# Kernel tuning notes

Hardware: AMD Instinct MI355X
Metric: run time of the kernel (lower is better)

Reference implementation:

```python
import jax, jax.numpy as jnp
import numpy as np

N_FEAT = 27  # 26 embeddings + bot MLP output
LI = np.array([i for i in range(N_FEAT) for j in range(i)])
LJ = np.array([j for i in range(N_FEAT) for j in range(i)])


def _mlp(x, Ws, bs):
    for W, b in zip(Ws, bs):
        x = jax.nn.relu(x @ W + b)
    return x


def setup_inputs() -> dict:
    key = jax.random.key(0)
    ks = jax.random.split(key, 32)
    B, V, D = 32768, 50000, 128
    bot = [13, 512, 256, 128]
    top = [479, 1024, 1024, 512, 256, 1]
    inp = {
        "dense_x": jax.random.normal(ks[0], (B, 13), dtype=jnp.float32),
        "sparse_x": jax.random.randint(ks[1], (B, 26), 0, V, dtype=jnp.int64),
        "emb": jax.random.normal(ks[2], (26, V, D), dtype=jnp.float32) * 0.01,
    }
    for i in range(3):
        inp[f"bw{i}"] = jax.random.normal(ks[3 + i], (bot[i], bot[i + 1]), dtype=jnp.float32) * (1.0 / np.sqrt(bot[i]))
        inp[f"bb{i}"] = jnp.zeros((bot[i + 1],), dtype=jnp.float32)
    for i in range(5):
        inp[f"tw{i}"] = jax.random.normal(ks[8 + i], (top[i], top[i + 1]), dtype=jnp.float32) * (1.0 / np.sqrt(top[i]))
        inp[f"tb{i}"] = jnp.zeros((top[i + 1],), dtype=jnp.float32)
    return inp


def reference(dense_x, sparse_x, emb,
              bw0, bb0, bw1, bb1, bw2, bb2,
              tw0, tb0, tw1, tb1, tw2, tb2, tw3, tb3, tw4, tb4):
    B = dense_x.shape[0]
    bot_out = _mlp(dense_x, [bw0, bw1, bw2], [bb0, bb1, bb2])  # [B, 128]
    # multi-table embedding gather: emb[t, sparse_x[:, t]] -> [B, 26, 128]
    gathered = jnp.take_along_axis(
        emb[None, :, :, :],  # broadcast over batch via vmap-style gather
        sparse_x.T[None, :, :, None].astype(jnp.int32) * 0, 0
    ) if False else jnp.stack(
        [emb[t][sparse_x[:, t]] for t in range(emb.shape[0])], axis=1
    )
    features = jnp.concatenate([bot_out[:, None, :], gathered], axis=1)  # [B, 27, 128]
    # batched dot interaction: [B, 27, 27], then triangular gather
    Z = jnp.einsum('bnd,bmd->bnm', features, features)
    interact = Z[:, LI, LJ]  # [B, 351]
    x = jnp.concatenate([bot_out, interact], axis=1)  # [B, 479]
    return _mlp(x, [tw0, tw1, tw2, tw3, tw4], [tb0, tb1, tb2, tb3, tb4])  # [B, 1]
```

## Files before the change

kernel.cpp:

```cpp
#include <hip/hip_runtime.h>

typedef _Float16 f16;
typedef __attribute__((ext_vector_type(2))) _Float16 f16x2;
typedef __attribute__((ext_vector_type(4))) _Float16 f16x4;
typedef __attribute__((ext_vector_type(8))) _Float16 f16x8;
typedef __attribute__((ext_vector_type(4))) float f32x4;

#define BM 128
#define BN 128
#define BK 32

#define TBM 256
#define TBN 256
#define TBK 64

__device__ __forceinline__ void gl_lds16(const void* g, void* l) {
    __builtin_amdgcn_global_load_lds(
        (const __attribute__((address_space(1))) void*)g,
        (__attribute__((address_space(3))) void*)l, 16, 0, 0);
}

struct ConvtDesc { const float* src; f16* dst; int K, N, Kpad, tileOff; };
struct ConvtArgs { ConvtDesc d[6]; };

__global__ void convt6_kernel(ConvtArgs args)
{
    __shared__ float tile[64][65];
    int bid = blockIdx.x;
    int w = 0;
    #pragma unroll
    for (int i = 1; i < 6; ++i) if (bid >= args.d[i].tileOff) w = i;
    const float* __restrict__ src = args.d[w].src;
    f16* __restrict__ dst = args.d[w].dst;
    int K = args.d[w].K, N = args.d[w].N, Kpad = args.d[w].Kpad;
    int local = bid - args.d[w].tileOff;
    int tk = Kpad >> 6;
    int k0 = (local % tk) * 64;
    int n0 = (local / tk) * 64;
    int tid = threadIdx.x;
    #pragma unroll
    for (int it = 0; it < 16; ++it) {
        int idx = it * 256 + tid;
        int kr = idx >> 6, nc = idx & 63;
        float v = 0.f;
        if (k0 + kr < K) v = src[(size_t)(k0 + kr) * N + n0 + nc];
        tile[kr][nc] = v;
    }
    __syncthreads();
    #pragma unroll
    for (int it = 0; it < 16; ++it) {
        int idx = it * 256 + tid;
        int nr = idx >> 6, kc = idx & 63;
        dst[(size_t)(n0 + nr) * Kpad + k0 + kc] = (f16)tile[kc][nr];
    }
}

__global__ void bot0_kernel(const float* __restrict__ xin, const float* __restrict__ w,
                            const float* __restrict__ bias, f16* __restrict__ out)
{
    int t = blockIdx.x * 256 + threadIdx.x;
    int b = t >> 9, n = t & 511;
    float acc = bias[n];
    #pragma unroll
    for (int k = 0; k < 13; ++k) acc += xin[b * 13 + k] * w[k * 512 + n];
    out[(size_t)b * 512 + n] = (f16)fmaxf(acc, 0.f);
}

__global__ void gemm_f16(const f16* __restrict__ A, const f16* __restrict__ WT,
                         const float* __restrict__ bias, f16* __restrict__ C,
                         int N, int K)
{
    __shared__ __align__(16) f16 lsA[BM * BK];
    __shared__ __align__(16) f16 lsB[BN * BK];
    int tid  = threadIdx.x;
    int lane = tid & 63;
    int wave = tid >> 6;
    int brow = blockIdx.y * BM;
    int bcol = blockIdx.x * BN;
    int wr = wave >> 1, wc = wave & 1;

    f32x4 acc[4][4] = {};
    int rsel = lane & 15;
    int k8   = lane >> 4;

    int nK = K / BK;
    for (int kt = 0; kt < nK; ++kt) {
        int k0 = kt * BK;
        #pragma unroll
        for (int i = 0; i < 2; ++i) {
            int flat = i * 256 + tid;
            int row  = flat >> 2;
            int slot = flat & 3;
            int sg   = slot ^ ((row >> 1) & 3);
            gl_lds16(A  + (size_t)(brow + row) * K + k0 + sg * 8, lsA + flat * 8);
            gl_lds16(WT + (size_t)(bcol + row) * K + k0 + sg * 8, lsB + flat * 8);
        }
        __syncthreads();

        f16x8 aF[4], bF[4];
        #pragma unroll
        for (int m = 0; m < 4; ++m) {
            int ra = wr * 64 + m * 16 + rsel;
            int sa = k8 ^ ((ra >> 1) & 3);
            aF[m] = *(const f16x8*)(lsA + ra * 32 + sa * 8);
        }
        #pragma unroll
        for (int n = 0; n < 4; ++n) {
            int rb = wc * 64 + n * 16 + rsel;
            int sb = k8 ^ ((rb >> 1) & 3);
            bF[n] = *(const f16x8*)(lsB + rb * 32 + sb * 8);
        }
        #pragma unroll
        for (int m = 0; m < 4; ++m)
            #pragma unroll
            for (int n = 0; n < 4; ++n)
                acc[m][n] = __builtin_amdgcn_mfma_f32_16x16x32_f16(aF[m], bF[n], acc[m][n], 0, 0, 0);
        __syncthreads();
    }

    #pragma unroll
    for (int n = 0; n < 4; ++n) {
        int col = bcol + wc * 64 + n * 16 + (lane & 15);
        float bv = bias[col];
        #pragma unroll
        for (int m = 0; m < 4; ++m) {
            int rowb = brow + wr * 64 + m * 16 + (lane >> 4) * 4;
            #pragma unroll
            for (int r = 0; r < 4; ++r) {
                float v = acc[m][n][r] + bv;
                C[(size_t)(rowb + r) * N + col] = (f16)fmaxf(v, 0.f);
            }
        }
    }
}

__global__ __launch_bounds__(512, 2) void gemm256_f16(
    const f16* __restrict__ A, const f16* __restrict__ WT,
    const float* __restrict__ bias, f16* __restrict__ C, int N, int K)
{
    __shared__ __align__(16) f16 ls[2][2 * TBM * TBK];
    int tid  = threadIdx.x;
    int lane = tid & 63;
    int wid  = tid >> 6;
    int wm = wid >> 2, wn = wid & 3;

    int nbx = gridDim.x;
    int flat = blockIdx.y * nbx + blockIdx.x;
    int nchunk = (nbx * gridDim.y) >> 3;
    int nf = (flat & 7) * nchunk + (flat >> 3);
    int bx = nf % nbx, by = nf / nbx;
    int brow = by * TBM, bcol = bx * TBN;

    f32x4 acc[8][4] = {};
    int rsel = lane & 15;
    int k8   = lane >> 4;

    const size_t szK = (size_t)K;
    auto stage = [&](int buf, int kt) {
        const f16* gA = A  + (size_t)brow * szK + kt * TBK;
        const f16* gB = WT + (size_t)bcol * szK + kt * TBK;
        f16* dA = &ls[buf][0];
        f16* dB = &ls[buf][TBM * TBK];
        #pragma unroll
        for (int i = 0; i < 4; ++i) {
            int fl  = i * 512 + tid;
            int row = fl >> 3;
            int sl  = fl & 7;
            int sg  = sl ^ (row & 7);
            gl_lds16(gA + (size_t)row * szK + sg * 8, dA + fl * 8);
            gl_lds16(gB + (size_t)row * szK + sg * 8, dB + fl * 8);
        }
    };

    int nK = K / TBK;
    stage(0, 0);
    __syncthreads();

    for (int kt = 0; kt < nK; ++kt) {
        int cur = kt & 1;
        if (kt + 1 < nK) stage(cur ^ 1, kt + 1);
        const f16* pA = &ls[cur][0];
        const f16* pB = &ls[cur][TBM * TBK];
        #pragma unroll
        for (int ks = 0; ks < 2; ++ks) {
            f16x8 aF[8], bF[4];
            #pragma unroll
            for (int m = 0; m < 8; ++m) {
                int ra = wm * 128 + m * 16 + rsel;
                int s  = (ks * 4 + k8) ^ (ra & 7);
                aF[m] = *(const f16x8*)(pA + ra * 64 + s * 8);
            }
            #pragma unroll
            for (int n = 0; n < 4; ++n) {
                int rb = wn * 64 + n * 16 + rsel;
                int s  = (ks * 4 + k8) ^ (rb & 7);
                bF[n] = *(const f16x8*)(pB + rb * 64 + s * 8);
            }
            #pragma unroll
            for (int m = 0; m < 8; ++m)
                #pragma unroll
                for (int n = 0; n < 4; ++n)
                    acc[m][n] = __builtin_amdgcn_mfma_f32_16x16x32_f16(aF[m], bF[n], acc[m][n], 0, 0, 0);
        }
        __syncthreads();
    }

    #pragma unroll
    for (int n = 0; n < 4; ++n) {
        int col = bcol + wn * 64 + n * 16 + (lane & 15);
        float bv = bias[col];
        #pragma unroll
        for (int m = 0; m < 8; ++m) {
            int rowb = brow + wm * 128 + m * 16 + (lane >> 4) * 4;
            #pragma unroll
            for (int r = 0; r < 4; ++r)
                C[(size_t)(rowb + r) * N + col] = (f16)fmaxf(acc[m][n][r] + bv, 0.f);
        }
    }
}

__global__ void interact_mfma(const f16* __restrict__ botout,
                              const float* __restrict__ emb,
                              const int* __restrict__ sparse,
                              f16* __restrict__ x, int V)
{
    __shared__ __align__(16) f16 F[4][32][128];
    __shared__ __align__(16) f16 xs[4][512];
    int tid  = threadIdx.x;
    int lane = tid & 63, wave = tid >> 6;
    int b0 = blockIdx.x * 4;

    for (int t = tid; t < 4 * 27 * 16; t += 256) {
        int s   = t / (27 * 16);
        int rem = t - s * (27 * 16);
        int r   = rem >> 4;
        int c   = rem & 15;
        int b   = b0 + s;
        f16x8 v;
        if (r == 0) {
            v = *(const f16x8*)(botout + (size_t)b * 128 + c * 8);
        } else {
            const float* src = emb + ((size_t)(r - 1) * V + sparse[b * 26 + (r - 1)]) * 128 + c * 8;
            #pragma unroll
            for (int e = 0; e < 8; ++e) v[e] = (f16)src[e];
        }
        *(f16x8*)(&F[s][r][(c ^ (r & 15)) * 8]) = v;
    }
    __syncthreads();

    f32x4 a00 = {}, a10 = {}, a11 = {};
    int rl = lane & 15, ch = lane >> 4;
    #pragma unroll
    for (int ks = 0; ks < 4; ++ks) {
        int c = ks * 4 + ch;
        f16x8 f0 = *(const f16x8*)(&F[wave][rl]     [(c ^ rl) * 8]);
        f16x8 f1 = *(const f16x8*)(&F[wave][16 + rl][(c ^ rl) * 8]);
        a00 = __builtin_amdgcn_mfma_f32_16x16x32_f16(f0, f0, a00, 0, 0, 0);
        a10 = __builtin_amdgcn_mfma_f32_16x16x32_f16(f1, f0, a10, 0, 0, 0);
        a11 = __builtin_amdgcn_mfma_f32_16x16x32_f16(f1, f1, a11, 0, 0, 0);
    }

    #pragma unroll
    for (int r = 0; r < 4; ++r) {
        int i = ch * 4 + r, j = rl;
        if (i > j) xs[wave][128 + (i * (i - 1)) / 2 + j] = (f16)a00[r];
    }
    #pragma unroll
    for (int r = 0; r < 4; ++r) {
        int i = 16 + ch * 4 + r, j = rl;
        if (i < 27) xs[wave][128 + (i * (i - 1)) / 2 + j] = (f16)a10[r];
    }
    #pragma unroll
    for (int r = 0; r < 4; ++r) {
        int i = 16 + ch * 4 + r, j = 16 + rl;
        if (i < 27 && j < i) xs[wave][128 + (i * (i - 1)) / 2 + j] = (f16)a11[r];
    }
    #pragma unroll
    for (int d = lane; d < 128; d += 64) xs[wave][d] = F[wave][0][d];
    if (lane < 33) xs[wave][479 + lane] = (f16)0;
    __syncthreads();

    {
        int b = b0 + wave;
        f16x8 v = *(const f16x8*)(&xs[wave][lane * 8]);
        *(f16x8*)(x + (size_t)b * 512 + lane * 8) = v;
    }
}

__global__ void top4_kernel(const f16* __restrict__ a, const float* __restrict__ w,
                            const float* __restrict__ bias, float* __restrict__ out)
{
    int wave = threadIdx.x >> 6, lane = threadIdx.x & 63;
    int b = blockIdx.x * 4 + wave;
    f16x4 av = *(const f16x4*)(a + (size_t)b * 256 + lane * 4);
    float acc = 0.f;
    #pragma unroll
    for (int k = 0; k < 4; ++k) acc += (float)av[k] * w[lane * 4 + k];
    #pragma unroll
    for (int off = 32; off; off >>= 1) acc += __shfl_xor(acc, off, 64);
    if (lane == 0) out[b] = fmaxf(acc + bias[0], 0.f);
}

extern "C" void kernel_launch(void* const* d_in, const int* in_sizes, int n_in,
                              void* d_out, int out_size, void* d_ws, size_t ws_size,
                              hipStream_t stream)
{
    (void)n_in; (void)out_size; (void)ws_size;
    const float* dense  = (const float*)d_in[0];
    const int*   sparse = (const int*)  d_in[1];
    const float* emb    = (const float*)d_in[2];
    const float* bw0 = (const float*)d_in[3];
    const float* bb0 = (const float*)d_in[4];
    const float* bw1 = (const float*)d_in[5];
    const float* bb1 = (const float*)d_in[6];
    const float* bw2 = (const float*)d_in[7];
    const float* bb2 = (const float*)d_in[8];
    const float* tw0 = (const float*)d_in[9];
    const float* tb0 = (const float*)d_in[10];
    const float* tw1 = (const float*)d_in[11];
    const float* tb1 = (const float*)d_in[12];
    const float* tw2 = (const float*)d_in[13];
    const float* tb2 = (const float*)d_in[14];
    const float* tw3 = (const float*)d_in[15];
    const float* tb3 = (const float*)d_in[16];
    const float* tw4 = (const float*)d_in[17];
    const float* tb4 = (const float*)d_in[18];
    float* out = (float*)d_out;

    const int B = in_sizes[0] / 13;
    const int V = in_sizes[2] / (26 * 128);

    char* ws = (char*)d_ws;
    size_t off = 0;
    auto alloc = [&](size_t bytes) {
        char* p = ws + off;
        off += (bytes + 255) & ~(size_t)255;
        return p;
    };
    f16* S1   = (f16*)alloc((size_t)B * 1024 * 2);
    f16* t1   = (f16*)alloc((size_t)B * 1024 * 2);
    f16* S3   = (f16*)alloc((size_t)B * 512 * 2);
    f16* S4   = (f16*)alloc((size_t)B * 256 * 2);
    f16* act2 = (f16*)alloc((size_t)B * 128 * 2);
    f16* bw1T = (f16*)alloc((size_t)256 * 512 * 2);
    f16* bw2T = (f16*)alloc((size_t)128 * 256 * 2);
    f16* tw0T = (f16*)alloc((size_t)1024 * 512 * 2);
    f16* tw1T = (f16*)alloc((size_t)1024 * 1024 * 2);
    f16* tw2T = (f16*)alloc((size_t)512 * 1024 * 2);
    f16* tw3T = (f16*)alloc((size_t)256 * 512 * 2);
    f16* act0 = S1; f16* t2 = S1;
    f16* x    = S3; f16* t3 = S3;
    f16* act1 = S4; f16* t4 = S4;

    ConvtArgs ca;
    ca.d[0] = { bw1, bw1T,  512,  256,  512,   0 };
    ca.d[1] = { bw2, bw2T,  256,  128,  256,  32 };
    ca.d[2] = { tw0, tw0T,  479, 1024,  512,  40 };
    ca.d[3] = { tw1, tw1T, 1024, 1024, 1024, 168 };
    ca.d[4] = { tw2, tw2T, 1024,  512, 1024, 424 };
    ca.d[5] = { tw3, tw3T,  512,  256,  512, 552 };
    convt6_kernel<<<584, 256, 0, stream>>>(ca);

    bot0_kernel<<<(B * 512) / 256, 256, 0, stream>>>(dense, bw0, bb0, act0);
    gemm_f16<<<dim3( 256/128, B/128), 256, 0, stream>>>(act0, bw1T, bb1, act1,  256,  512);
    gemm_f16<<<dim3( 128/128, B/128), 256, 0, stream>>>(act1, bw2T, bb2, act2,  128,  256);
    interact_mfma<<<B / 4, 256, 0, stream>>>(act2, emb, sparse, x, V);
    gemm256_f16<<<dim3(1024/256, B/256), 512, 0, stream>>>(x,  tw0T, tb0, t1, 1024,  512);
    gemm256_f16<<<dim3(1024/256, B/256), 512, 0, stream>>>(t1, tw1T, tb1, t2, 1024, 1024);
    gemm256_f16<<<dim3( 512/256, B/256), 512, 0, stream>>>(t2, tw2T, tb2, t3,  512, 1024);
    gemm_f16<<<dim3( 256/128, B/128), 256, 0, stream>>>(t3, tw3T, tb3, t4,  256,  512);
    top4_kernel<<<B / 4, 256, 0, stream>>>(t4, tw4, tb4, out);
}
```

Baseline: 397.9 us.

## Double-buffer small GEMM and use partial vmcnt waits with setprio in both GEMMs

The 128x128 GEMM gets double-buffered LDS so the next K tile's global-to-LDS loads are issued before computing on the current tile. Both GEMM kernels replace __syncthreads with an explicit partial s_waitcnt vmcnt plus s_barrier, so the wait covers only the current tile's loads and the prefetch stays in flight. MFMA sections are wrapped in s_setprio to favor compute waves. The cost is double the LDS in the small GEMM, which may reduce occupancy. The hand-written vmcnt counts must match the exact number of loads issued per stage, so they are fragile.

```diff
diff --git a/kernel.cpp b/kernel.cpp
--- a/kernel.cpp
+++ b/kernel.cpp
@@ -70,8 +70,8 @@
                          const float* __restrict__ bias, f16* __restrict__ C,
                          int N, int K)
 {
-    __shared__ __align__(16) f16 lsA[BM * BK];
-    __shared__ __align__(16) f16 lsB[BN * BK];
+    __shared__ __align__(16) f16 lsA[2][BM * BK];
+    __shared__ __align__(16) f16 lsB[2][BN * BK];
     int tid  = threadIdx.x;
     int lane = tid & 63;
     int wave = tid >> 6;
@@ -83,8 +83,7 @@
     int rsel = lane & 15;
     int k8   = lane >> 4;
 
-    int nK = K / BK;
-    for (int kt = 0; kt < nK; ++kt) {
+    auto stage = [&](int buf, int kt) {
         int k0 = kt * BK;
         #pragma unroll
         for (int i = 0; i < 2; ++i) {
@@ -92,30 +91,44 @@
             int row  = flat >> 2;
             int slot = flat & 3;
             int sg   = slot ^ ((row >> 1) & 3);
-            gl_lds16(A  + (size_t)(brow + row) * K + k0 + sg * 8, lsA + flat * 8);
-            gl_lds16(WT + (size_t)(bcol + row) * K + k0 + sg * 8, lsB + flat * 8);
-        }
-        __syncthreads();
-
+            gl_lds16(A  + (size_t)(brow + row) * K + k0 + sg * 8, lsA[buf] + flat * 8);
+            gl_lds16(WT + (size_t)(bcol + row) * K + k0 + sg * 8, lsB[buf] + flat * 8);
+        }
+    };
+
+    int nK = K / BK;
+    stage(0, 0);
+    for (int kt = 0; kt < nK; ++kt) {
+        int cur = kt & 1;
+        if (kt + 1 < nK) {
+            stage(cur ^ 1, kt + 1);
+            asm volatile("s_waitcnt vmcnt(4)" ::: "memory");
+        } else {
+            asm volatile("s_waitcnt vmcnt(0)" ::: "memory");
+        }
+        __builtin_amdgcn_s_barrier();
+
+        __builtin_amdgcn_s_setprio(1);
         f16x8 aF[4], bF[4];
         #pragma unroll
         for (int m = 0; m < 4; ++m) {
             int ra = wr * 64 + m * 16 + rsel;
             int sa = k8 ^ ((ra >> 1) & 3);
-            aF[m] = *(const f16x8*)(lsA + ra * 32 + sa * 8);
+            aF[m] = *(const f16x8*)(lsA[cur] + ra * 32 + sa * 8);
         }
         #pragma unroll
         for (int n = 0; n < 4; ++n) {
             int rb = wc * 64 + n * 16 + rsel;
             int sb = k8 ^ ((rb >> 1) & 3);
-            bF[n] = *(const f16x8*)(lsB + rb * 32 + sb * 8);
+            bF[n] = *(const f16x8*)(lsB[cur] + rb * 32 + sb * 8);
         }
         #pragma unroll
         for (int m = 0; m < 4; ++m)
             #pragma unroll
             for (int n = 0; n < 4; ++n)
                 acc[m][n] = __builtin_amdgcn_mfma_f32_16x16x32_f16(aF[m], bF[n], acc[m][n], 0, 0, 0);
-        __syncthreads();
+        __builtin_amdgcn_s_setprio(0);
+        __builtin_amdgcn_s_barrier();
     }
 
     #pragma unroll
@@ -174,13 +187,19 @@
 
     int nK = K / TBK;
     stage(0, 0);
-    __syncthreads();
-
     for (int kt = 0; kt < nK; ++kt) {
         int cur = kt & 1;
-        if (kt + 1 < nK) stage(cur ^ 1, kt + 1);
+        if (kt + 1 < nK) {
+            stage(cur ^ 1, kt + 1);
+            asm volatile("s_waitcnt vmcnt(8)" ::: "memory");
+        } else {
+            asm volatile("s_waitcnt vmcnt(0)" ::: "memory");
+        }
+        __builtin_amdgcn_s_barrier();
+
         const f16* pA = &ls[cur][0];
         const f16* pB = &ls[cur][TBM * TBK];
+        __builtin_amdgcn_s_setprio(1);
         #pragma unroll
         for (int ks = 0; ks < 2; ++ks) {
             f16x8 aF[8], bF[4];
@@ -202,7 +221,8 @@
                 for (int n = 0; n < 4; ++n)
                     acc[m][n] = __builtin_amdgcn_mfma_f32_16x16x32_f16(aF[m], bF[n], acc[m][n], 0, 0, 0);
         }
-        __syncthreads();
+        __builtin_amdgcn_s_setprio(0);
+        __builtin_amdgcn_s_barrier();
     }
 
     #pragma unroll
```

After: 407.0 us. 2.3% more time.
